# Kernel optimization log

Measured on AMD Instinct MI355X. Metric: run time of the kernel, lower is better.

The kernel has to match this reference:

```python
import jax, jax.numpy as jnp
import numpy as np
import math

DIM_V = 512

def setup_inputs() -> dict:
    key = jax.random.key(0)
    k1, k2, k3, k4, k5, k6 = jax.random.split(key, 6)
    B, C, N, M = 8, DIM_V, 4096, 1024
    pcd_up = jax.random.normal(k1, (B, C, N), dtype=jnp.float32)
    pcd_down = jax.random.normal(k2, (B, C, M), dtype=jnp.float32)
    s = 1.0 / math.sqrt(C)
    Wq = jax.random.normal(k3, (C, C), dtype=jnp.float32) * s
    Wk = jax.random.normal(k4, (C, C), dtype=jnp.float32) * s
    Wv = jax.random.normal(k5, (C, C), dtype=jnp.float32) * s
    Wskip = jax.random.normal(k6, (C, C), dtype=jnp.float32) * s
    return {"pcd_up": pcd_up, "pcd_down": pcd_down, "Wq": Wq, "Wk": Wk, "Wv": Wv, "Wskip": Wskip}

def reference(pcd_up, pcd_down, Wq, Wk, Wv, Wskip):
    # 1x1 Conv1d == per-point linear: weight [out_c, in_c]
    q = jnp.einsum('oc,bcn->bon', Wq, pcd_up)      # [B, C, N]
    k = jnp.einsum('oc,bcm->bom', Wk, pcd_down)    # [B, C, M]
    v = jnp.einsum('oc,bcm->bom', Wv, pcd_down)    # [B, C, M]
    C = q.shape[1]
    scale = jnp.sqrt(jnp.asarray(C, dtype=q.dtype))  # sqrt(q.shape[-2]) = sqrt(C)
    energy = jnp.einsum('bcn,bcm->bnm', q, k) / scale  # [B, N, M]
    attention = jax.nn.softmax(energy, axis=-1)
    x = jnp.einsum('bnm,bcm->bcn', attention, v)       # [B, C, N]
    skip = jnp.einsum('oc,bcn->bon', Wskip, pcd_up)
    return skip + x
```

## Files before the change

### kernel.cpp

```cpp
#include <hip/hip_runtime.h>
#include <cstddef>

#define Bn 8
#define Cd 512
#define Nn 4096
#define Mm 1024

typedef __attribute__((ext_vector_type(8))) short s8v;
typedef __attribute__((ext_vector_type(4))) float v4f;
typedef __attribute__((ext_vector_type(16))) float v16f;

__device__ __forceinline__ float b2f(unsigned short u) {
    union { unsigned int i; float f; } v; v.i = ((unsigned int)u) << 16; return v.f;
}
__device__ __forceinline__ unsigned short f2b(float f) {
    union { float f; unsigned int i; } v; v.f = f;
    unsigned int x = v.i;
    unsigned int r = (x + 0x7FFFu + ((x >> 16) & 1u)) >> 16;
    return (unsigned short)r;
}
__device__ __forceinline__ unsigned int f2b2(float lo, float hi) {
    return (unsigned int)f2b(lo) | ((unsigned int)f2b(hi) << 16);
}
__device__ __forceinline__ v4f mfma16(s8v a, s8v b, v4f c) {
    return __builtin_amdgcn_mfma_f32_16x16x32_bf16(a, b, c, 0, 0, 0);
}
__device__ __forceinline__ v16f mfma32(s8v a, s8v b, v16f c) {
    return __builtin_amdgcn_mfma_f32_32x32x16_bf16(a, b, c, 0, 0, 0);
}

__global__ __launch_bounds__(256) void convwf(const float* __restrict__ Wq, const float* __restrict__ Wk,
                                              const float* __restrict__ Wv, const float* __restrict__ Ws,
                                              unsigned short* __restrict__ Wf) {
    const float* S = (blockIdx.y == 0) ? Wq : (blockIdx.y == 1) ? Wk : (blockIdx.y == 2) ? Wv : Ws;
    const int o16 = blockIdx.x;
    const int t = threadIdx.x;
    const int l = t & 63, sub = t >> 6;
    const int lq = l & 15, quad = l >> 4;
    unsigned short* dst = Wf + (size_t)blockIdx.y * 262144;
#pragma unroll
    for (int rep = 0; rep < 4; ++rep) {
        int cstep = sub * 4 + rep;
        const float* src = S + (size_t)(o16 * 16 + lq) * Cd + cstep * 32 + quad * 8;
        float4 va = *(const float4*)(src);
        float4 vb = *(const float4*)(src + 4);
        union { ushort4 h[2]; uint4 q; } pk;
        pk.h[0].x = f2b(va.x); pk.h[0].y = f2b(va.y); pk.h[0].z = f2b(va.z); pk.h[0].w = f2b(va.w);
        pk.h[1].x = f2b(vb.x); pk.h[1].y = f2b(vb.y); pk.h[1].z = f2b(vb.z); pk.h[1].w = f2b(vb.w);
        *(uint4*)(dst + ((size_t)(o16 * 16 + cstep) * 64 + l) * 8) = pk.q;
    }
}

__global__ __launch_bounds__(256, 2) void gemm_kv(const unsigned short* __restrict__ Wf,
                                                  const float* __restrict__ down,
                                                  unsigned short* __restrict__ Kf,
                                                  unsigned short* __restrict__ Vf) {
    __shared__ __align__(16) unsigned char raw[37888];
    const int t = threadIdx.x;
    const int l = t & 63, w = t >> 6, lq = t & 15, quad = (t >> 4) & 3;
    const int bid = blockIdx.x;
    const int b = bid & 7, mt = (bid >> 3) & 31, half = bid >> 8;
    const int m0 = mt * 32;
    const float* db = down + (size_t)b * Cd * Mm + m0;
    const unsigned short* W1f = Wf + (size_t)1 * 262144 + (size_t)l * 8;
    const unsigned short* W2f = Wf + (size_t)2 * 262144 + (size_t)l * 8;

    {
#pragma unroll
        for (int rep = 0; rep < 8; ++rep) {
            int u = rep * 256 + t;
            int c2 = u >> 3, m4 = (u & 7) * 4;
            float4 a = *(const float4*)(db + (size_t)(2 * c2) * Mm + m4);
            float4 c = *(const float4*)(db + (size_t)(2 * c2 + 1) * Mm + m4);
            int cu = c2 >> 2, sb = (c2 & 3) * 4;
            float av[4] = {a.x, a.y, a.z, a.w};
            float cv[4] = {c.x, c.y, c.z, c.w};
#pragma unroll
            for (int j = 0; j < 4; ++j) {
                int m = m4 + j;
                *(unsigned int*)(raw + ((m * 64 + (cu ^ (m & 15))) << 4) + sb) = f2b2(av[j], cv[j]);
            }
        }
    }
    __syncthreads();

    v4f acc1[4][2], acc2[4][2];
#pragma unroll
    for (int i = 0; i < 4; ++i)
#pragma unroll
        for (int nt = 0; nt < 2; ++nt) {
            acc1[i][nt] = (v4f){0.f, 0.f, 0.f, 0.f};
            acc2[i][nt] = (v4f){0.f, 0.f, 0.f, 0.f};
        }

    for (int step = 0; step < 16; ++step) {
        s8v a1[4], a2[4];
#pragma unroll
        for (int i = 0; i < 4; ++i) {
            int o16 = half * 16 + w * 4 + i;
            a1[i] = *(const s8v*)(W1f + ((size_t)(o16 * 16 + step) << 9));
            a2[i] = *(const s8v*)(W2f + ((size_t)(o16 * 16 + step) << 9));
        }
        s8v bf0 = *(const s8v*)(raw + ((lq * 64 + ((step * 4 + quad) ^ lq)) << 4));
        s8v bf1 = *(const s8v*)(raw + (((lq + 16) * 64 + ((step * 4 + quad) ^ lq)) << 4));
#pragma unroll
        for (int i = 0; i < 4; ++i) {
            acc1[i][0] = mfma16(a1[i], bf0, acc1[i][0]);
            acc1[i][1] = mfma16(a1[i], bf1, acc1[i][1]);
            acc2[i][0] = mfma16(a2[i], bf0, acc2[i][0]);
            acc2[i][1] = mfma16(a2[i], bf1, acc2[i][1]);
        }
    }
    __syncthreads();

    const int hq = quad >> 1, ebase = (quad & 1) * 4;
    {
        unsigned short* Kb = Kf + (size_t)b * Mm * Cd;
#pragma unroll
        for (int i = 0; i < 4; ++i) {
            int kb = half * 16 + w * 4 + i;
#pragma unroll
            for (int nt = 0; nt < 2; ++nt) {
                int lf = (nt * 16 + lq) + 32 * hq;
                ushort4 v;
                v.x = f2b(acc1[i][nt][0]); v.y = f2b(acc1[i][nt][1]);
                v.z = f2b(acc1[i][nt][2]); v.w = f2b(acc1[i][nt][3]);
                *(ushort4*)(Kb + ((size_t)(mt * 32 + kb) * 64 + lf) * 8 + ebase) = v;
            }
        }
    }
    short (*Vst)[40] = reinterpret_cast<short(*)[40]>(raw + 32768 + w * 1280);
    unsigned short* Vb0 = Vf + (size_t)b * Cd * Mm;
#pragma unroll
    for (int i = 0; i < 4; ++i) {
        int o16 = half * 16 + w * 4 + i;
#pragma unroll
        for (int nt = 0; nt < 2; ++nt)
#pragma unroll
            for (int r = 0; r < 4; ++r)
                Vst[quad * 4 + r][nt * 16 + lq] = (short)f2b(acc2[i][nt][r]);
        int c_abs = o16 * 16 + (l >> 2);
        int m8 = l & 3;
        int ct = c_abs >> 5, mb = (m0 >> 4) + (m8 >> 1);
        int lf = (c_abs & 31) + 32 * (m8 & 1);
        uint4 v = *(const uint4*)(&Vst[l >> 2][m8 * 8]);
        *(uint4*)(Vb0 + ((size_t)(ct * 64 + mb) * 64 + lf) * 8) = v;
    }
}

template <int MODE>
__global__ __launch_bounds__(256) void gemm_mfma(const float* __restrict__ W,
                                                 const float* __restrict__ X,
                                                 float* __restrict__ Yf,
                                                 unsigned short* __restrict__ Yb,
                                                 int Nx) {
    __shared__ short Xs[64][40];
    __shared__ short Tt[16][72];
    const int t = threadIdx.x;
    const int w = t >> 6, lq = t & 15, quad = (t >> 4) & 3;
    const int b = blockIdx.z, o0 = blockIdx.y * 64, n0 = blockIdx.x * 64;
    const float* Xb = X + (size_t)b * Cd * Nx;
    const float* Wrow = W + (size_t)(o0 + w * 16 + lq) * Cd;

    v4f acc[4];
#pragma unroll
    for (int i = 0; i < 4; ++i) acc[i] = (v4f){0.f, 0.f, 0.f, 0.f};

    for (int c0 = 0; c0 < Cd; c0 += 32) {
#pragma unroll
        for (int p = 0; p < 2; ++p) {
            int i = t + p * 256;
            int c = i >> 4;
            int n4 = (i & 15) * 4;
            float4 x = *(const float4*)(Xb + (size_t)(c0 + c) * Nx + n0 + n4);
            Xs[n4 + 0][c] = (short)f2b(x.x); Xs[n4 + 1][c] = (short)f2b(x.y);
            Xs[n4 + 2][c] = (short)f2b(x.z); Xs[n4 + 3][c] = (short)f2b(x.w);
        }
        union { unsigned short h[8]; s8v s; } af;
        {
            float4 wa = *(const float4*)(Wrow + c0 + quad * 8);
            float4 wb = *(const float4*)(Wrow + c0 + quad * 8 + 4);
            af.h[0] = f2b(wa.x); af.h[1] = f2b(wa.y); af.h[2] = f2b(wa.z); af.h[3] = f2b(wa.w);
            af.h[4] = f2b(wb.x); af.h[5] = f2b(wb.y); af.h[6] = f2b(wb.z); af.h[7] = f2b(wb.w);
        }
        __syncthreads();
#pragma unroll
        for (int nt = 0; nt < 4; ++nt) {
            s8v bf = *(const s8v*)(&Xs[nt * 16 + lq][quad * 8]);
            acc[nt] = mfma16(af.s, bf, acc[nt]);
        }
        __syncthreads();
    }

    if (MODE == 0) {
#pragma unroll
        for (int nt = 0; nt < 4; ++nt)
#pragma unroll
            for (int r = 0; r < 4; ++r) {
                int o = o0 + w * 16 + quad * 4 + r;
                int n = n0 + nt * 16 + lq;
                Yf[((size_t)b * Cd + o) * Nx + n] = acc[nt][r];
            }
    } else {
#pragma unroll
        for (int nt = 0; nt < 4; ++nt) {
#pragma unroll
            for (int r = 0; r < 4; ++r)
                Tt[lq][w * 16 + quad * 4 + r] = (short)f2b(acc[nt][r]);
            __syncthreads();
            int nrow = t >> 4, o4 = (t & 15) * 4;
            ushort4 val = *(const ushort4*)(&Tt[nrow][o4]);
            *(ushort4*)(Yb + ((size_t)b * Nx + n0 + nt * 16 + nrow) * Cd + o0 + o4) = val;
            __syncthreads();
        }
    }
}

__global__ __launch_bounds__(512, 2) void attn_f(const float* __restrict__ up,
                                                 const unsigned short* __restrict__ Wf,
                                                 const unsigned short* __restrict__ Kf,
                                                 const unsigned short* __restrict__ Vf,
                                                 float* __restrict__ out) {
    __shared__ __align__(16) unsigned char Ls[104192];
    unsigned char* Lq = Ls;
    unsigned short* Pb = (unsigned short*)(Ls + 65536);
    float* pmaxS  = (float*)(Ls + 99328);
    float* psumS  = (float*)(Ls + 101376);
    float* muS    = (float*)(Ls + 103424);
    float* ssumS  = (float*)(Ls + 103680);
    float* alphaS = (float*)(Ls + 103936);
    float* OtA    = (float*)Ls;

    const int t = threadIdx.x;
    const int l = t & 63, w = t >> 6;
    const int lcol = l & 31, lhalf = l >> 5;
    const int lq = l & 15, quad = (l >> 4) & 3;
    const int bid = blockIdx.x;
    const int b = bid & 7, n0 = (bid >> 3) * 64;

    {
        const float* ub = up + (size_t)b * Cd * Nn + n0;
#pragma unroll
        for (int it = 0; it < 8; ++it) {
            int u = it * 512 + t;
            int c2 = u >> 4, n4 = (u & 15) * 4;
            float4 a = *(const float4*)(ub + (size_t)(2 * c2) * Nn + n4);
            float4 c = *(const float4*)(ub + (size_t)(2 * c2 + 1) * Nn + n4);
            int cu = c2 >> 2, sb = (c2 & 3) * 4;
            float av[4] = {a.x, a.y, a.z, a.w};
            float cv[4] = {c.x, c.y, c.z, c.w};
#pragma unroll
            for (int j = 0; j < 4; ++j) {
                int n = n4 + j;
                *(unsigned int*)(Lq + ((n * 64 + (cu ^ (n & 15))) << 4) + sb) = f2b2(av[j], cv[j]);
            }
        }
    }
    __syncthreads();

    {
        v4f aq[4][4], ask[4][4];
#pragma unroll
        for (int oi = 0; oi < 4; ++oi)
#pragma unroll
            for (int ni = 0; ni < 4; ++ni) {
                aq[oi][ni] = (v4f){0.f, 0.f, 0.f, 0.f};
                ask[oi][ni] = (v4f){0.f, 0.f, 0.f, 0.f};
            }
        const unsigned short* WqF = Wf + (size_t)l * 8;
        const unsigned short* WsF = Wf + (size_t)3 * 262144 + (size_t)l * 8;
        for (int step = 0; step < 16; ++step) {
            s8v a1[4], a2[4];
#pragma unroll
            for (int oi = 0; oi < 4; ++oi)
                a1[oi] = *(const s8v*)(WqF + ((size_t)((w * 4 + oi) * 16 + step) << 9));
#pragma unroll
            for (int oi = 0; oi < 4; ++oi)
                a2[oi] = *(const s8v*)(WsF + ((size_t)((w * 4 + oi) * 16 + step) << 9));
#pragma unroll
            for (int ni = 0; ni < 4; ++ni) {
                int n = ni * 16 + lq;
                s8v bf = *(const s8v*)(Lq + ((n * 64 + ((step * 4 + quad) ^ lq)) << 4));
#pragma unroll
                for (int oi = 0; oi < 4; ++oi) {
                    aq[oi][ni] = mfma16(a1[oi], bf, aq[oi][ni]);
                    ask[oi][ni] = mfma16(a2[oi], bf, ask[oi][ni]);
                }
            }
        }
#pragma unroll
        for (int oi = 0; oi < 4; ++oi)
#pragma unroll
            for (int ni = 0; ni < 4; ++ni)
#pragma unroll
                for (int r = 0; r < 4; ++r) {
                    int o = w * 64 + oi * 16 + quad * 4 + r;
                    int n = n0 + ni * 16 + lq;
                    out[((size_t)b * Cd + o) * Nn + n] = ask[oi][ni][r];
                }
        __syncthreads();
#pragma unroll
        for (int oi = 0; oi < 4; ++oi)
#pragma unroll
            for (int ni = 0; ni < 4; ++ni) {
                int n = ni * 16 + lq;
                int cu = w * 8 + oi * 2 + (quad >> 1);
                ushort4 pk;
                pk.x = f2b(aq[oi][ni][0]); pk.y = f2b(aq[oi][ni][1]);
                pk.z = f2b(aq[oi][ni][2]); pk.w = f2b(aq[oi][ni][3]);
                *(ushort4*)(Lq + ((n * 64 + (cu ^ lq)) << 4) + (quad & 1) * 8) = pk;
            }
    }
    if (t < 64) { muS[t] = -1e30f; ssumS[t] = 0.f; }

    v16f o_acc[2][2];
#pragma unroll
    for (int nh = 0; nh < 2; ++nh)
#pragma unroll
        for (int ti = 0; ti < 2; ++ti)
#pragma unroll
            for (int r = 0; r < 16; ++r) o_acc[nh][ti][r] = 0.f;
    __syncthreads();

    const unsigned short* Kfb = Kf + (size_t)b * Mm * Cd + (size_t)l * 8;
    const unsigned short* Vfb = Vf + (size_t)b * Cd * Mm + (size_t)l * 8;
    const int q0 = lcol * 64, q1 = (lcol + 32) * 64;
    const int swz = lcol & 15;
    const float sc = 0.04419417382415922f;

    for (int m0 = 0; m0 < Mm; m0 += 256) {
        v16f st0, st1;
#pragma unroll
        for (int r = 0; r < 16; ++r) { st0[r] = 0.f; st1[r] = 0.f; }
        const unsigned short* kp = Kfb + (size_t)(((m0 >> 5) + w) * 32) * 512;
#pragma unroll
        for (int kb8 = 0; kb8 < 4; ++kb8) {
            uint4 ka[8];
#pragma unroll
            for (int j = 0; j < 8; ++j) ka[j] = *(const uint4*)(kp + (size_t)(kb8 * 8 + j) * 512);
            __builtin_amdgcn_s_setprio(1);
#pragma unroll
            for (int j = 0; j < 8; ++j) {
                int kb = kb8 * 8 + j;
                int uo = (kb * 2 + lhalf) ^ swz;
                s8v qf0 = *(const s8v*)(Lq + ((q0 + uo) << 4));
                s8v qf1 = *(const s8v*)(Lq + ((q1 + uo) << 4));
                union { uint4 u; s8v s; } av; av.u = ka[j];
                st0 = mfma32(av.s, qf0, st0);
                st1 = mfma32(av.s, qf1, st1);
            }
            __builtin_amdgcn_s_setprio(0);
        }
        uint4 v0p[8];
        {
            const unsigned short* vc = Vfb + (size_t)((w * 2) * 64 + (m0 >> 4)) * 512;
#pragma unroll
            for (int j = 0; j < 8; ++j) v0p[j] = *(const uint4*)(vc + (size_t)j * 512);
        }
#pragma unroll
        for (int r = 0; r < 16; ++r) { st0[r] *= sc; st1[r] *= sc; }
        float tm0 = st0[0], tm1 = st1[0];
#pragma unroll
        for (int r = 1; r < 16; ++r) { tm0 = fmaxf(tm0, st0[r]); tm1 = fmaxf(tm1, st1[r]); }
        tm0 = fmaxf(tm0, __shfl_xor(tm0, 32));
        tm1 = fmaxf(tm1, __shfl_xor(tm1, 32));
        if (l < 32) {
            pmaxS[l * 8 + w] = tm0;
            pmaxS[(l + 32) * 8 + w] = tm1;
        }
        __syncthreads();
        {
            int row = t >> 3, p = t & 7;
            float v = pmaxS[row * 8 + p];
            v = fmaxf(v, __shfl_xor(v, 1));
            v = fmaxf(v, __shfl_xor(v, 2));
            v = fmaxf(v, __shfl_xor(v, 4));
            if (p == 0) {
                float mold = muS[row];
                float mx = fmaxf(mold, v);
                alphaS[row] = __expf(mold - mx);
                muS[row] = mx;
            }
        }
        __syncthreads();
        {
            float mx0 = muS[lcol], mx1 = muS[lcol + 32];
            float e0[16], e1[16], rs0 = 0.f, rs1 = 0.f;
#pragma unroll
            for (int r = 0; r < 16; ++r) {
                e0[r] = __expf(st0[r] - mx0); rs0 += e0[r];
                e1[r] = __expf(st1[r] - mx1); rs1 += e1[r];
            }
            rs0 += __shfl_xor(rs0, 32);
            rs1 += __shfl_xor(rs1, 32);
            if (l < 32) {
                psumS[l * 8 + w] = rs0;
                psumS[(l + 32) * 8 + w] = rs1;
            }
#pragma unroll
            for (int rg = 0; rg < 4; ++rg) {
                ushort4 pk0, pk1;
                pk0.x = f2b(e0[rg * 4 + 0]); pk0.y = f2b(e0[rg * 4 + 1]);
                pk0.z = f2b(e0[rg * 4 + 2]); pk0.w = f2b(e0[rg * 4 + 3]);
                pk1.x = f2b(e1[rg * 4 + 0]); pk1.y = f2b(e1[rg * 4 + 1]);
                pk1.z = f2b(e1[rg * 4 + 2]); pk1.w = f2b(e1[rg * 4 + 3]);
                *(ushort4*)(Pb + lcol * 264 + w * 32 + 8 * rg + 4 * lhalf) = pk0;
                *(ushort4*)(Pb + (lcol + 32) * 264 + w * 32 + 8 * rg + 4 * lhalf) = pk1;
            }
        }
        __syncthreads();
        {
            int row = t >> 3, p = t & 7;
            float v = psumS[row * 8 + p];
            v += __shfl_xor(v, 1);
            v += __shfl_xor(v, 2);
            v += __shfl_xor(v, 4);
            if (p == 0) ssumS[row] = ssumS[row] * alphaS[row] + v;
        }

        float ar0[16], ar1[16];
#pragma unroll
        for (int r = 0; r < 16; ++r) {
            int crow = (r & 3) + 8 * (r >> 2) + 4 * lhalf;
            ar0[r] = alphaS[crow];
            ar1[r] = alphaS[32 + crow];
        }
#pragma unroll
        for (int ti = 0; ti < 2; ++ti)
#pragma unroll
            for (int r = 0; r < 16; ++r) {
                o_acc[0][ti][r] *= ar0[r];
                o_acc[1][ti][r] *= ar1[r];
            }

#pragma unroll
        for (int h = 0; h < 2; ++h) {
            s8v pA0[8], pA1[8];
#pragma unroll
            for (int j = 0; j < 8; ++j) {
                pA0[j] = *(const s8v*)(Pb + lcol * 264 + (h * 8 + j) * 16 + lhalf * 8);
                pA1[j] = *(const s8v*)(Pb + (lcol + 32) * 264 + (h * 8 + j) * 16 + lhalf * 8);
            }
#pragma unroll
            for (int ti = 0; ti < 2; ++ti) {
                uint4 vb[8];
                if (h == 0 && ti == 0) {
#pragma unroll
                    for (int j = 0; j < 8; ++j) vb[j] = v0p[j];
                } else {
                    const unsigned short* vc = Vfb + (size_t)((w * 2 + ti) * 64 + (m0 >> 4) + h * 8) * 512;
#pragma unroll
                    for (int j = 0; j < 8; ++j) vb[j] = *(const uint4*)(vc + (size_t)j * 512);
                }
                __builtin_amdgcn_s_setprio(1);
#pragma unroll
                for (int j = 0; j < 8; ++j) {
                    union { uint4 u; s8v s; } bv; bv.u = vb[j];
                    o_acc[0][ti] = mfma32(pA0[j], bv.s, o_acc[0][ti]);
                    o_acc[1][ti] = mfma32(pA1[j], bv.s, o_acc[1][ti]);
                }
                __builtin_amdgcn_s_setprio(0);
            }
        }
        __syncthreads();
    }

    float inv0[16], inv1[16];
#pragma unroll
    for (int r = 0; r < 16; ++r) {
        int crow = (r & 3) + 8 * (r >> 2) + 4 * lhalf;
        inv0[r] = 1.0f / ssumS[crow];
        inv1[r] = 1.0f / ssumS[32 + crow];
    }
    float* OtW = OtA + w * 32 * 36;
#pragma unroll
    for (int nh = 0; nh < 2; ++nh)
#pragma unroll
        for (int ti = 0; ti < 2; ++ti) {
#pragma unroll
            for (int r = 0; r < 16; ++r) {
                int crow = (r & 3) + 8 * (r >> 2) + 4 * lhalf;
                OtW[lcol * 36 + crow] = o_acc[nh][ti][r] * (nh ? inv1[r] : inv0[r]);
            }
            int cloc = l >> 1, half = l & 1;
            int cabs = (w * 2 + ti) * 32 + cloc;
            const float* src = OtW + cloc * 36 + half * 16;
            float* op = out + ((size_t)b * Cd + cabs) * Nn + n0 + nh * 32 + half * 16;
#pragma unroll
            for (int j = 0; j < 4; ++j) {
                float4 a = *(const float4*)(src + j * 4);
                float4 g = *(const float4*)(op + j * 4);
                g.x += a.x; g.y += a.y; g.z += a.z; g.w += a.w;
                *(float4*)(op + j * 4) = g;
            }
        }
}

__device__ __forceinline__ float u2lo(unsigned int u) {
    union { unsigned int i; float f; } v; v.i = u << 16; return v.f;
}
__device__ __forceinline__ float u2hi(unsigned int u) {
    union { unsigned int i; float f; } v; v.i = u & 0xFFFF0000u; return v.f;
}

__global__ __launch_bounds__(256) void attn_k(const float* __restrict__ up,
                                              const float* __restrict__ Wq,
                                              const unsigned short* __restrict__ Ktb,
                                              const unsigned short* __restrict__ Vtb,
                                              float* __restrict__ out) {
    __shared__ float Qs[16][516];
    __shared__ __align__(16) unsigned char Sraw[24576];
    unsigned short (*Us)[16]  = reinterpret_cast<unsigned short(*)[16]>(Sraw);
    unsigned short (*Wt)[512] = reinterpret_cast<unsigned short(*)[512]>(Sraw + 16384);
    float (*Ps)[65] = reinterpret_cast<float(*)[65]>(Sraw);
    float* mu_s     = reinterpret_cast<float*>(Sraw + 4160);
    float* ssum_s   = reinterpret_cast<float*>(Sraw + 4224);
    float* alpha_s  = reinterpret_cast<float*>(Sraw + 4288);

    const int t = threadIdx.x;
    const int b = blockIdx.y;
    const int n0 = blockIdx.x * 16;
    const int row = t & 15;
    const int grp = t >> 4;

    for (int i = t; i < Cd * 16; i += 256) {
        int c = i >> 4, r = i & 15;
        Us[c][r] = f2b(up[((size_t)b * Cd + c) * Nn + n0 + r]);
    }
    __syncthreads();

    float acc[32];
#pragma unroll
    for (int j = 0; j < 32; ++j) acc[j] = 0.f;

    for (int k0 = 0; k0 < Cd; k0 += 8) {
        for (int i = t; i < 1024; i += 256) {
            int oc = i >> 1;
            int kc = (i & 1) * 4;
            float4 wv = *(const float4*)(Wq + (size_t)oc * Cd + k0 + kc);
            Wt[kc + 0][oc] = f2b(wv.x); Wt[kc + 1][oc] = f2b(wv.y);
            Wt[kc + 2][oc] = f2b(wv.z); Wt[kc + 3][oc] = f2b(wv.w);
        }
        __syncthreads();
#pragma unroll
        for (int k = 0; k < 8; ++k) {
            float u = b2f(Us[k0 + k][row]);
            const ushort4* wr = (const ushort4*)(&Wt[k][grp * 32]);
#pragma unroll
            for (int j4 = 0; j4 < 8; ++j4) {
                ushort4 wv = wr[j4];
                acc[j4 * 4 + 0] += u * b2f(wv.x);
                acc[j4 * 4 + 1] += u * b2f(wv.y);
                acc[j4 * 4 + 2] += u * b2f(wv.z);
                acc[j4 * 4 + 3] += u * b2f(wv.w);
            }
        }
        __syncthreads();
    }

    const float scale = 0.04419417382415922f;
#pragma unroll
    for (int j = 0; j < 32; ++j) Qs[row][grp * 32 + j] = acc[j] * scale;
    if (t < 16) { mu_s[t] = -1e30f; ssum_s[t] = 0.f; }
#pragma unroll
    for (int j = 0; j < 32; ++j) acc[j] = 0.f;
    __syncthreads();

    const float4* qr = (const float4*)(&Qs[row][0]);

    for (int m0 = 0; m0 < Mm; m0 += 64) {
        {
            int mb = m0 + grp * 4;
            const uint4* K0 = (const uint4*)(Ktb + ((size_t)b * Mm + mb + 0) * Cd);
            const uint4* K1 = (const uint4*)(Ktb + ((size_t)b * Mm + mb + 1) * Cd);
            const uint4* K2 = (const uint4*)(Ktb + ((size_t)b * Mm + mb + 2) * Cd);
            const uint4* K3 = (const uint4*)(Ktb + ((size_t)b * Mm + mb + 3) * Cd);
            float a0 = 0.f, a1 = 0.f, a2 = 0.f, a3 = 0.f;
#pragma unroll 4
            for (int c8 = 0; c8 < Cd / 8; ++c8) {
                float4 qa = qr[2 * c8], qb = qr[2 * c8 + 1];
                uint4 k0v = K0[c8], k1v = K1[c8], k2v = K2[c8], k3v = K3[c8];
                a0 += qa.x * u2lo(k0v.x) + qa.y * u2hi(k0v.x) + qa.z * u2lo(k0v.y) + qa.w * u2hi(k0v.y)
                    + qb.x * u2lo(k0v.z) + qb.y * u2hi(k0v.z) + qb.z * u2lo(k0v.w) + qb.w * u2hi(k0v.w);
                a1 += qa.x * u2lo(k1v.x) + qa.y * u2hi(k1v.x) + qa.z * u2lo(k1v.y) + qa.w * u2hi(k1v.y)
                    + qb.x * u2lo(k1v.z) + qb.y * u2hi(k1v.z) + qb.z * u2lo(k1v.w) + qb.w * u2hi(k1v.w);
                a2 += qa.x * u2lo(k2v.x) + qa.y * u2hi(k2v.x) + qa.z * u2lo(k2v.y) + qa.w * u2hi(k2v.y)
                    + qb.x * u2lo(k2v.z) + qb.y * u2hi(k2v.z) + qb.z * u2lo(k2v.w) + qb.w * u2hi(k2v.w);
                a3 += qa.x * u2lo(k3v.x) + qa.y * u2hi(k3v.x) + qa.z * u2lo(k3v.y) + qa.w * u2hi(k3v.y)
                    + qb.x * u2lo(k3v.z) + qb.y * u2hi(k3v.z) + qb.z * u2lo(k3v.w) + qb.w * u2hi(k3v.w);
            }
            Ps[row][grp * 4 + 0] = a0;
            Ps[row][grp * 4 + 1] = a1;
            Ps[row][grp * 4 + 2] = a2;
            Ps[row][grp * 4 + 3] = a3;
        }
        __syncthreads();
        if (t < 16) {
            float mold = mu_s[t];
            float mx = mold;
            for (int m = 0; m < 64; ++m) mx = fmaxf(mx, Ps[t][m]);
            float al = __expf(mold - mx);
            float s = ssum_s[t] * al;
            for (int m = 0; m < 64; ++m) {
                float p = __expf(Ps[t][m] - mx);
                Ps[t][m] = p;
                s += p;
            }
            mu_s[t] = mx; ssum_s[t] = s; alpha_s[t] = al;
        }
        __syncthreads();
        {
            float arr = alpha_s[row];
#pragma unroll
            for (int j = 0; j < 32; ++j) acc[j] *= arr;
            const unsigned short* Vbase = Vtb + (size_t)b * Mm * Cd + (size_t)grp * 32;
            for (int m = 0; m < 64; ++m) {
                float p = Ps[row][m];
                const uint4* vr = (const uint4*)(Vbase + (size_t)(m0 + m) * Cd);
#pragma unroll
                for (int j4 = 0; j4 < 4; ++j4) {
                    uint4 v = vr[j4];
                    acc[j4 * 8 + 0] += p * u2lo(v.x); acc[j4 * 8 + 1] += p * u2hi(v.x);
                    acc[j4 * 8 + 2] += p * u2lo(v.y); acc[j4 * 8 + 3] += p * u2hi(v.y);
                    acc[j4 * 8 + 4] += p * u2lo(v.z); acc[j4 * 8 + 5] += p * u2hi(v.z);
                    acc[j4 * 8 + 6] += p * u2lo(v.w); acc[j4 * 8 + 7] += p * u2hi(v.w);
                }
            }
        }
        __syncthreads();
    }

    float invv = 1.0f / ssum_s[row];
#pragma unroll
    for (int j = 0; j < 32; ++j) {
        int c = grp * 32 + j;
        size_t idx = ((size_t)b * Cd + c) * Nn + n0 + row;
        out[idx] = out[idx] + acc[j] * invv;
    }
}

extern "C" void kernel_launch(void* const* d_in, const int* in_sizes, int n_in,
                              void* d_out, int out_size, void* d_ws, size_t ws_size,
                              hipStream_t stream) {
    const float* up   = (const float*)d_in[0];
    const float* down = (const float*)d_in[1];
    const float* Wq   = (const float*)d_in[2];
    const float* Wk   = (const float*)d_in[3];
    const float* Wv   = (const float*)d_in[4];
    const float* Wsk  = (const float*)d_in[5];
    float* out = (float*)d_out;

    const size_t szK = (size_t)Bn * Mm * Cd;
    const size_t szW = (size_t)4 * Cd * Cd;

    if (ws_size >= (2 * szK + szW) * 2) {
        unsigned short* Kf = (unsigned short*)d_ws;
        unsigned short* Vf = Kf + szK;
        unsigned short* Wf = Vf + szK;
        convwf<<<dim3(32, 4), 256, 0, stream>>>(Wq, Wk, Wv, Wsk, Wf);
        gemm_kv<<<dim3(Bn * (Mm / 32) * 2), 256, 0, stream>>>(Wf, down, Kf, Vf);
        attn_f<<<dim3((Nn / 64) * Bn), 512, 0, stream>>>(up, Wf, Kf, Vf, out);
    } else {
        unsigned short* Ktb = (unsigned short*)d_ws;
        unsigned short* Vtb = Ktb + szK;
        gemm_mfma<2><<<dim3(Mm / 64, Cd / 64, Bn), 256, 0, stream>>>(Wk, down, nullptr, Ktb, Mm);
        gemm_mfma<2><<<dim3(Mm / 64, Cd / 64, Bn), 256, 0, stream>>>(Wv, down, nullptr, Vtb, Mm);
        gemm_mfma<0><<<dim3(Nn / 64, Cd / 64, Bn), 256, 0, stream>>>(Wsk, up, out, nullptr, Nn);
        attn_k<<<dim3(Nn / 16, Bn), 256, 0, stream>>>(up, Wq, Ktb, Vtb, out);
    }
}
```

Before: 272.9 us.

## Use 1024-thread attention blocks with 16 waves splitting keys and channels

Doubles the fused attention block from 8 to 16 waves. Each wave now computes half as many output channels in the Q/skip projection, scores 32 keys of a 512-key tile (twice the previous tile width), and accumulates one 32-channel slice of the output. The aim is to halve per-wave register accumulators and the number of online-softmax iterations while raising the wave count per block. In exchange, shared memory grows to about 138 KB, so only one block fits per CU, and the cross-wave max/sum reductions gain an extra shuffle stage.

```diff
diff --git a/kernel.cpp b/kernel.cpp
--- a/kernel.cpp
+++ b/kernel.cpp
@@ -216,19 +216,19 @@
     }
 }
 
-__global__ __launch_bounds__(512, 2) void attn_f(const float* __restrict__ up,
-                                                 const unsigned short* __restrict__ Wf,
-                                                 const unsigned short* __restrict__ Kf,
-                                                 const unsigned short* __restrict__ Vf,
-                                                 float* __restrict__ out) {
-    __shared__ __align__(16) unsigned char Ls[104192];
+__global__ __launch_bounds__(1024) void attn_f(const float* __restrict__ up,
+                                               const unsigned short* __restrict__ Wf,
+                                               const unsigned short* __restrict__ Kf,
+                                               const unsigned short* __restrict__ Vf,
+                                               float* __restrict__ out) {
+    __shared__ __align__(16) unsigned char Ls[141056];
     unsigned char* Lq = Ls;
     unsigned short* Pb = (unsigned short*)(Ls + 65536);
-    float* pmaxS  = (float*)(Ls + 99328);
-    float* psumS  = (float*)(Ls + 101376);
-    float* muS    = (float*)(Ls + 103424);
-    float* ssumS  = (float*)(Ls + 103680);
-    float* alphaS = (float*)(Ls + 103936);
+    float* pmaxS  = (float*)(Ls + 132096);
+    float* psumS  = (float*)(Ls + 136192);
+    float* muS    = (float*)(Ls + 140288);
+    float* ssumS  = (float*)(Ls + 140544);
+    float* alphaS = (float*)(Ls + 140800);
     float* OtA    = (float*)Ls;
 
     const int t = threadIdx.x;
@@ -241,8 +241,8 @@
     {
         const float* ub = up + (size_t)b * Cd * Nn + n0;
 #pragma unroll
-        for (int it = 0; it < 8; ++it) {
-            int u = it * 512 + t;
+        for (int it = 0; it < 4; ++it) {
+            int u = it * 1024 + t;
             int c2 = u >> 4, n4 = (u & 15) * 4;
             float4 a = *(const float4*)(ub + (size_t)(2 * c2) * Nn + n4);
             float4 c = *(const float4*)(ub + (size_t)(2 * c2 + 1) * Nn + n4);
@@ -259,9 +259,9 @@
     __syncthreads();
 
     {
-        v4f aq[4][4], ask[4][4];
-#pragma unroll
-        for (int oi = 0; oi < 4; ++oi)
+        v4f aq[2][4], ask[2][4];
+#pragma unroll
+        for (int oi = 0; oi < 2; ++oi)
 #pragma unroll
             for (int ni = 0; ni < 4; ++ni) {
                 aq[oi][ni] = (v4f){0.f, 0.f, 0.f, 0.f};
@@ -270,41 +270,40 @@
         const unsigned short* WqF = Wf + (size_t)l * 8;
         const unsigned short* WsF = Wf + (size_t)3 * 262144 + (size_t)l * 8;
         for (int step = 0; step < 16; ++step) {
-            s8v a1[4], a2[4];
-#pragma unroll
-            for (int oi = 0; oi < 4; ++oi)
-                a1[oi] = *(const s8v*)(WqF + ((size_t)((w * 4 + oi) * 16 + step) << 9));
-#pragma unroll
-            for (int oi = 0; oi < 4; ++oi)
-                a2[oi] = *(const s8v*)(WsF + ((size_t)((w * 4 + oi) * 16 + step) << 9));
+            s8v a1[2], a2[2];
+#pragma unroll
+            for (int oi = 0; oi < 2; ++oi) {
+                a1[oi] = *(const s8v*)(WqF + ((size_t)((w * 2 + oi) * 16 + step) << 9));
+                a2[oi] = *(const s8v*)(WsF + ((size_t)((w * 2 + oi) * 16 + step) << 9));
+            }
 #pragma unroll
             for (int ni = 0; ni < 4; ++ni) {
                 int n = ni * 16 + lq;
                 s8v bf = *(const s8v*)(Lq + ((n * 64 + ((step * 4 + quad) ^ lq)) << 4));
 #pragma unroll
-                for (int oi = 0; oi < 4; ++oi) {
+                for (int oi = 0; oi < 2; ++oi) {
                     aq[oi][ni] = mfma16(a1[oi], bf, aq[oi][ni]);
                     ask[oi][ni] = mfma16(a2[oi], bf, ask[oi][ni]);
                 }
             }
         }
 #pragma unroll
-        for (int oi = 0; oi < 4; ++oi)
+        for (int oi = 0; oi < 2; ++oi)
 #pragma unroll
             for (int ni = 0; ni < 4; ++ni)
 #pragma unroll
                 for (int r = 0; r < 4; ++r) {
-                    int o = w * 64 + oi * 16 + quad * 4 + r;
+                    int o = w * 32 + oi * 16 + quad * 4 + r;
                     int n = n0 + ni * 16 + lq;
                     out[((size_t)b * Cd + o) * Nn + n] = ask[oi][ni][r];
                 }
         __syncthreads();
 #pragma unroll
-        for (int oi = 0; oi < 4; ++oi)
+        for (int oi = 0; oi < 2; ++oi)
 #pragma unroll
             for (int ni = 0; ni < 4; ++ni) {
                 int n = ni * 16 + lq;
-                int cu = w * 8 + oi * 2 + (quad >> 1);
+                int cu = w * 4 + oi * 2 + (quad >> 1);
                 ushort4 pk;
                 pk.x = f2b(aq[oi][ni][0]); pk.y = f2b(aq[oi][ni][1]);
                 pk.z = f2b(aq[oi][ni][2]); pk.w = f2b(aq[oi][ni][3]);
@@ -313,13 +312,11 @@
     }
     if (t < 64) { muS[t] = -1e30f; ssumS[t] = 0.f; }
 
-    v16f o_acc[2][2];
+    v16f o_acc[2];
 #pragma unroll
     for (int nh = 0; nh < 2; ++nh)
 #pragma unroll
-        for (int ti = 0; ti < 2; ++ti)
-#pragma unroll
-            for (int r = 0; r < 16; ++r) o_acc[nh][ti][r] = 0.f;
+        for (int r = 0; r < 16; ++r) o_acc[nh][r] = 0.f;
     __syncthreads();
 
     const unsigned short* Kfb = Kf + (size_t)b * Mm * Cd + (size_t)l * 8;
@@ -328,7 +325,7 @@
     const int swz = lcol & 15;
     const float sc = 0.04419417382415922f;
 
-    for (int m0 = 0; m0 < Mm; m0 += 256) {
+    for (int m0 = 0; m0 < Mm; m0 += 512) {
         v16f st0, st1;
 #pragma unroll
         for (int r = 0; r < 16; ++r) { st0[r] = 0.f; st1[r] = 0.f; }
@@ -353,7 +350,7 @@
         }
         uint4 v0p[8];
         {
-            const unsigned short* vc = Vfb + (size_t)((w * 2) * 64 + (m0 >> 4)) * 512;
+            const unsigned short* vc = Vfb + (size_t)(w * 64 + (m0 >> 4)) * 512;
 #pragma unroll
             for (int j = 0; j < 8; ++j) v0p[j] = *(const uint4*)(vc + (size_t)j * 512);
         }
@@ -365,16 +362,17 @@
         tm0 = fmaxf(tm0, __shfl_xor(tm0, 32));
         tm1 = fmaxf(tm1, __shfl_xor(tm1, 32));
         if (l < 32) {
-            pmaxS[l * 8 + w] = tm0;
-            pmaxS[(l + 32) * 8 + w] = tm1;
+            pmaxS[l * 16 + w] = tm0;
+            pmaxS[(l + 32) * 16 + w] = tm1;
         }
         __syncthreads();
         {
-            int row = t >> 3, p = t & 7;
-            float v = pmaxS[row * 8 + p];
+            int row = t >> 4, p = t & 15;
+            float v = pmaxS[row * 16 + p];
             v = fmaxf(v, __shfl_xor(v, 1));
             v = fmaxf(v, __shfl_xor(v, 2));
             v = fmaxf(v, __shfl_xor(v, 4));
+            v = fmaxf(v, __shfl_xor(v, 8));
             if (p == 0) {
                 float mold = muS[row];
                 float mx = fmaxf(mold, v);
@@ -394,8 +392,8 @@
             rs0 += __shfl_xor(rs0, 32);
             rs1 += __shfl_xor(rs1, 32);
             if (l < 32) {
-                psumS[l * 8 + w] = rs0;
-                psumS[(l + 32) * 8 + w] = rs1;
+                psumS[l * 16 + w] = rs0;
+                psumS[(l + 32) * 16 + w] = rs1;
             }
 #pragma unroll
             for (int rg = 0; rg < 4; ++rg) {
@@ -404,17 +402,18 @@
                 pk0.z = f2b(e0[rg * 4 + 2]); pk0.w = f2b(e0[rg * 4 + 3]);
                 pk1.x = f2b(e1[rg * 4 + 0]); pk1.y = f2b(e1[rg * 4 + 1]);
                 pk1.z = f2b(e1[rg * 4 + 2]); pk1.w = f2b(e1[rg * 4 + 3]);
-                *(ushort4*)(Pb + lcol * 264 + w * 32 + 8 * rg + 4 * lhalf) = pk0;
-                *(ushort4*)(Pb + (lcol + 32) * 264 + w * 32 + 8 * rg + 4 * lhalf) = pk1;
+                *(ushort4*)(Pb + lcol * 520 + w * 32 + 8 * rg + 4 * lhalf) = pk0;
+                *(ushort4*)(Pb + (lcol + 32) * 520 + w * 32 + 8 * rg + 4 * lhalf) = pk1;
             }
         }
         __syncthreads();
         {
-            int row = t >> 3, p = t & 7;
-            float v = psumS[row * 8 + p];
+            int row = t >> 4, p = t & 15;
+            float v = psumS[row * 16 + p];
             v += __shfl_xor(v, 1);
             v += __shfl_xor(v, 2);
             v += __shfl_xor(v, 4);
+            v += __shfl_xor(v, 8);
             if (p == 0) ssumS[row] = ssumS[row] * alphaS[row] + v;
         }
 
@@ -426,41 +425,33 @@
             ar1[r] = alphaS[32 + crow];
         }
 #pragma unroll
-        for (int ti = 0; ti < 2; ++ti)
-#pragma unroll
-            for (int r = 0; r < 16; ++r) {
-                o_acc[0][ti][r] *= ar0[r];
-                o_acc[1][ti][r] *= ar1[r];
-            }
-
-#pragma unroll
-        for (int h = 0; h < 2; ++h) {
-            s8v pA0[8], pA1[8];
+        for (int r = 0; r < 16; ++r) {
+            o_acc[0][r] *= ar0[r];
+            o_acc[1][r] *= ar1[r];
+        }
+
+#pragma unroll
+        for (int g = 0; g < 4; ++g) {
+            uint4 vb[8];
+            if (g == 0) {
+#pragma unroll
+                for (int j = 0; j < 8; ++j) vb[j] = v0p[j];
+            } else {
+                const unsigned short* vc = Vfb + (size_t)(w * 64 + (m0 >> 4) + g * 8) * 512;
+#pragma unroll
+                for (int j = 0; j < 8; ++j) vb[j] = *(const uint4*)(vc + (size_t)j * 512);
+            }
+            __builtin_amdgcn_s_setprio(1);
 #pragma unroll
             for (int j = 0; j < 8; ++j) {
-                pA0[j] = *(const s8v*)(Pb + lcol * 264 + (h * 8 + j) * 16 + lhalf * 8);
-                pA1[j] = *(const s8v*)(Pb + (lcol + 32) * 264 + (h * 8 + j) * 16 + lhalf * 8);
-            }
-#pragma unroll
-            for (int ti = 0; ti < 2; ++ti) {
-                uint4 vb[8];
-                if (h == 0 && ti == 0) {
-#pragma unroll
-                    for (int j = 0; j < 8; ++j) vb[j] = v0p[j];
-                } else {
-                    const unsigned short* vc = Vfb + (size_t)((w * 2 + ti) * 64 + (m0 >> 4) + h * 8) * 512;
-#pragma unroll
-                    for (int j = 0; j < 8; ++j) vb[j] = *(const uint4*)(vc + (size_t)j * 512);
-                }
-                __builtin_amdgcn_s_setprio(1);
-#pragma unroll
-                for (int j = 0; j < 8; ++j) {
-                    union { uint4 u; s8v s; } bv; bv.u = vb[j];
-                    o_acc[0][ti] = mfma32(pA0[j], bv.s, o_acc[0][ti]);
-                    o_acc[1][ti] = mfma32(pA1[j], bv.s, o_acc[1][ti]);
-                }
-                __builtin_amdgcn_s_setprio(0);
-            }
+                int kb = g * 8 + j;
+                s8v pA0 = *(const s8v*)(Pb + lcol * 520 + kb * 16 + lhalf * 8);
+                s8v pA1 = *(const s8v*)(Pb + (lcol + 32) * 520 + kb * 16 + lhalf * 8);
+                union { uint4 u; s8v s; } bv; bv.u = vb[j];
+                o_acc[0] = mfma32(pA0, bv.s, o_acc[0]);
+                o_acc[1] = mfma32(pA1, bv.s, o_acc[1]);
+            }
+            __builtin_amdgcn_s_setprio(0);
         }
         __syncthreads();
     }
@@ -474,26 +465,24 @@
     }
     float* OtW = OtA + w * 32 * 36;
 #pragma unroll
-    for (int nh = 0; nh < 2; ++nh)
-#pragma unroll
-        for (int ti = 0; ti < 2; ++ti) {
-#pragma unroll
-            for (int r = 0; r < 16; ++r) {
-                int crow = (r & 3) + 8 * (r >> 2) + 4 * lhalf;
-                OtW[lcol * 36 + crow] = o_acc[nh][ti][r] * (nh ? inv1[r] : inv0[r]);
-            }
-            int cloc = l >> 1, half = l & 1;
-            int cabs = (w * 2 + ti) * 32 + cloc;
-            const float* src = OtW + cloc * 36 + half * 16;
-            float* op = out + ((size_t)b * Cd + cabs) * Nn + n0 + nh * 32 + half * 16;
-#pragma unroll
-            for (int j = 0; j < 4; ++j) {
-                float4 a = *(const float4*)(src + j * 4);
-                float4 g = *(const float4*)(op + j * 4);
-                g.x += a.x; g.y += a.y; g.z += a.z; g.w += a.w;
-                *(float4*)(op + j * 4) = g;
-            }
-        }
+    for (int nh = 0; nh < 2; ++nh) {
+#pragma unroll
+        for (int r = 0; r < 16; ++r) {
+            int crow = (r & 3) + 8 * (r >> 2) + 4 * lhalf;
+            OtW[lcol * 36 + crow] = o_acc[nh][r] * (nh ? inv1[r] : inv0[r]);
+        }
+        int cloc = l >> 1, half = l & 1;
+        int cabs = w * 32 + cloc;
+        const float* src = OtW + cloc * 36 + half * 16;
+        float* op = out + ((size_t)b * Cd + cabs) * Nn + n0 + nh * 32 + half * 16;
+#pragma unroll
+        for (int j = 0; j < 4; ++j) {
+            float4 a = *(const float4*)(src + j * 4);
+            float4 g = *(const float4*)(op + j * 4);
+            g.x += a.x; g.y += a.y; g.z += a.z; g.w += a.w;
+            *(float4*)(op + j * 4) = g;
+        }
+    }
 }
 
 __device__ __forceinline__ float u2lo(unsigned int u) {
@@ -659,7 +648,7 @@
         unsigned short* Wf = Vf + szK;
         convwf<<<dim3(32, 4), 256, 0, stream>>>(Wq, Wk, Wv, Wsk, Wf);
         gemm_kv<<<dim3(Bn * (Mm / 32) * 2), 256, 0, stream>>>(Wf, down, Kf, Vf);
-        attn_f<<<dim3((Nn / 64) * Bn), 512, 0, stream>>>(up, Wf, Kf, Vf, out);
+        attn_f<<<dim3((Nn / 64) * Bn), 1024, 0, stream>>>(up, Wf, Kf, Vf, out);
     } else {
         unsigned short* Ktb = (unsigned short*)d_ws;
         unsigned short* Vtb = Ktb + szK;
```

After: 383.7 us. 1.41x slower.
